# Kernel optimization log

Hardware: AMD Instinct MI355X
Metric: run time of the kernel (lower is better)

## Reference

```python
import jax, jax.numpy as jnp
import numpy as np
import math

B, N, HID, NH = 128, 512, 512, 8
DH = HID // NH  # d_heads = 64


def setup_inputs() -> dict:
    key = jax.random.key(0)
    ks = jax.random.split(key, 8)
    s = 0.05  # keep logits in a sane range
    h = jax.random.normal(ks[0], (B, N, HID), dtype=jnp.float32)
    lengths = jax.random.randint(ks[1], (B,), 1, N + 1, dtype=jnp.int32)
    w_q = jax.random.normal(ks[2], (HID, HID), dtype=jnp.float32) * s
    w_k = jax.random.normal(ks[3], (HID, HID), dtype=jnp.float32) * s
    w_v = jax.random.normal(ks[4], (HID, HID), dtype=jnp.float32) * s
    w_o = jax.random.normal(ks[5], (HID, HID), dtype=jnp.float32) * s
    w_seed_w = jax.random.normal(ks[6], (HID, 1), dtype=jnp.float32) * s  # Linear(1, k*hidden), k=1
    w_seed_b = jax.random.normal(ks[7], (HID,), dtype=jnp.float32) * s
    seed_vec = jnp.ones((1,), dtype=jnp.float32)
    return {"h": h, "lengths": lengths, "w_q": w_q, "w_k": w_k, "w_v": w_v,
            "w_o": w_o, "w_seed_w": w_seed_w, "w_seed_b": w_seed_b, "seed_vec": seed_vec}


def reference(h, lengths, w_q, w_k, w_v, w_o, w_seed_w, w_seed_b, seed_vec):
    # PMA with k=1 seed query. norm_features=False.
    # query = w_seed(seed_vec), same for every graph in the batch.
    query = w_seed_w @ seed_vec + w_seed_b            # [HID]
    q = (w_q @ query).reshape(NH, DH)                 # [NH, DH] (Linear: x @ W.T == W @ x for vector)
    # NOTE: original code computes w_k(v) but never uses it in attention; output
    # depends only on q and v (e = q * v summed over d_heads). We skip the dead compute.
    v = (h @ w_v.T).reshape(B, N, NH, DH)             # [B, N, NH, DH]
    # logits: e[b,h,n] = <q[h], v[b,n,h]> / sqrt(DH)
    e = jnp.einsum("hd,bnhd->bhn", q, v) / math.sqrt(DH)
    valid = jnp.arange(N)[None, :] < lengths[:, None]  # [B, N] ragged mask
    e = jnp.where(valid[:, None, :], e, -jnp.inf)
    alpha = jax.nn.softmax(e, axis=-1)                # [B, NH, N]; padded cols -> 0
    out_h = jnp.einsum("bhn,bnhd->bhd", alpha, v)     # [B, NH, DH]
    out = out_h.reshape(B, HID) @ w_o.T               # [B*k, HID], packed (k=1)
    alpha_out = alpha[..., None]                      # [B, NH, N, 1] matching torch permute
    return out, alpha_out
```

## Files before the change

### kernel.cpp

```cpp
#include <hip/hip_runtime.h>
#include <math.h>

constexpr int B = 128, N = 512, HID = 512, NH = 8, DH = 64;

__global__ __launch_bounds__(64) void k1_qk(
    const float* __restrict__ w_q, const float* __restrict__ w_v,
    const float* __restrict__ w_sw, const float* __restrict__ w_sb,
    const float* __restrict__ seed, float* __restrict__ qk)
{
    __shared__ __align__(16) float query_s[HID];
    __shared__ float q_s[DH];
    const int t  = threadIdx.x;
    const int h  = blockIdx.x >> 3;
    const int jc = blockIdx.x & 7;
    const float sv = seed[0];
    #pragma unroll
    for (int k = 0; k < 8; ++k) {
        const int j = t * 8 + k;
        query_s[j] = w_sw[j] * sv + w_sb[j];
    }
    __syncthreads();
    {
        const float* row = w_q + (size_t)(h * DH + t) * HID;
        float acc = 0.f;
        for (int j = 0; j < HID; j += 4) {
            const float4 wv = *(const float4*)(row + j);
            acc += wv.x * query_s[j]     + wv.y * query_s[j + 1]
                 + wv.z * query_s[j + 2] + wv.w * query_s[j + 3];
        }
        q_s[t] = acc;
    }
    __syncthreads();
    {
        const int j = jc * 64 + t;
        float acc = 0.f;
        for (int d = 0; d < DH; ++d)
            acc += q_s[d] * w_v[(size_t)(h * DH + d) * HID + j];
        qk[h * HID + j] = acc * 0.125f;
    }
}

__global__ __launch_bounds__(256) void ke_logits(
    const float* __restrict__ hbuf, const int* __restrict__ lengths,
    const float* __restrict__ qk, float* __restrict__ e_ws)
{
    const int t = threadIdx.x;
    const int l = t & 63;
    const int w = t >> 6;
    const int b = blockIdx.x >> 3;
    const int c = blockIdx.x & 7;
    const int n0 = c * 64;
    const int len = lengths[b];
    if (n0 >= len) return;

    float4 qlo[NH], qhi[NH];
    #pragma unroll
    for (int hh = 0; hh < NH; ++hh) {
        qlo[hh] = *(const float4*)&qk[hh * HID + l * 4];
        qhi[hh] = *(const float4*)&qk[hh * HID + 256 + l * 4];
    }

    const int nmax = min(n0 + 64, len);
    const float* hb = hbuf + (size_t)b * N * HID;
    const int hh_out = ((l & 1) << 2) | (l & 2) | ((l >> 2) & 1);

    for (int n = n0 + w; n < nmax; n += 4) {
        const float* row = hb + (size_t)n * HID;
        const float4 h0 = *(const float4*)(row + l * 4);
        const float4 h1 = *(const float4*)(row + 256 + l * 4);
        float v[NH];
        #pragma unroll
        for (int hh = 0; hh < NH; ++hh)
            v[hh] = h0.x * qlo[hh].x + h0.y * qlo[hh].y
                  + h0.z * qlo[hh].z + h0.w * qlo[hh].w
                  + h1.x * qhi[hh].x + h1.y * qhi[hh].y
                  + h1.z * qhi[hh].z + h1.w * qhi[hh].w;

        #pragma unroll
        for (int i = 0; i < 4; ++i) {
            const float ax = __shfl_xor(v[i], 1, 64);
            const float bx = __shfl_xor(v[i + 4], 1, 64);
            v[i] = (l & 1) ? (v[i + 4] + bx) : (v[i] + ax);
        }
        #pragma unroll
        for (int i = 0; i < 2; ++i) {
            const float ax = __shfl_xor(v[i], 2, 64);
            const float bx = __shfl_xor(v[i + 2], 2, 64);
            v[i] = (l & 2) ? (v[i + 2] + bx) : (v[i] + ax);
        }
        {
            const float ax = __shfl_xor(v[0], 4, 64);
            const float bx = __shfl_xor(v[1], 4, 64);
            v[0] = (l & 4) ? (v[1] + bx) : (v[0] + ax);
        }
        v[0] += __shfl_xor(v[0], 8, 64);
        v[0] += __shfl_xor(v[0], 16, 64);
        v[0] += __shfl_xor(v[0], 32, 64);

        if (l < 8)
            e_ws[(size_t)(b * NH + hh_out) * N + n] = v[0];
    }
}

__global__ __launch_bounds__(256) void ks_softmax(
    const float* __restrict__ e_ws, const int* __restrict__ lengths,
    float* __restrict__ alpha, float* __restrict__ al_t)
{
    const int b    = blockIdx.x >> 1;
    const int grp  = blockIdx.x & 1;
    const int lane = threadIdx.x & 63;
    const int hh   = grp * 4 + (threadIdx.x >> 6);
    const int len  = lengths[b];

    const float* e = e_ws + (size_t)(b * NH + hh) * N;
    float ev[8];
    float m = -3.0e38f;
    #pragma unroll
    for (int it = 0; it < 8; ++it) {
        const int n = it * 64 + lane;
        ev[it] = (n < len) ? e[n] : -3.0e38f;
        m = fmaxf(m, ev[it]);
    }
    #pragma unroll
    for (int off = 32; off; off >>= 1)
        m = fmaxf(m, __shfl_xor(m, off, 64));
    float s = 0.f;
    #pragma unroll
    for (int it = 0; it < 8; ++it) {
        ev[it] = __expf(ev[it] - m);
        s += ev[it];
    }
    #pragma unroll
    for (int off = 32; off; off >>= 1)
        s += __shfl_xor(s, off, 64);
    const float inv = 1.f / s;
    float* ao = alpha + (size_t)(b * NH + hh) * N;
    float* at = al_t + (size_t)b * N * NH + hh;
    #pragma unroll
    for (int it = 0; it < 8; ++it) {
        const int n   = it * 64 + lane;
        const float v = (n < len) ? ev[it] * inv : 0.f;
        ao[n]      = v;
        at[n * NH] = v;
    }
}

__global__ __launch_bounds__(256) void kc_ctx(
    const float* __restrict__ hbuf, const int* __restrict__ lengths,
    const float* __restrict__ al_t, float* __restrict__ ctxp)
{
    const int t   = threadIdx.x;
    const int b   = blockIdx.x >> 3;
    const int c   = blockIdx.x & 7;
    const int n0  = c * 64;
    const int g   = t >> 7;
    const int cq  = t & 127;
    const int len = lengths[b];
    const int nend = min(len - n0, 64);

    float4 acc[NH];
    #pragma unroll
    for (int hh = 0; hh < NH; ++hh) { acc[hh].x = acc[hh].y = acc[hh].z = acc[hh].w = 0.f; }

    const float* hb = hbuf + ((size_t)b * N + n0) * HID + cq * 4;
    const float* ap = al_t + ((size_t)b * N + n0) * NH;
    #pragma unroll 4
    for (int ln = g; ln < nend; ln += 2) {
        const float4 hv = *(const float4*)(hb + (size_t)ln * HID);
        const float* a = ap + ln * NH;
        acc[0].x += a[0] * hv.x; acc[0].y += a[0] * hv.y; acc[0].z += a[0] * hv.z; acc[0].w += a[0] * hv.w;
        acc[1].x += a[1] * hv.x; acc[1].y += a[1] * hv.y; acc[1].z += a[1] * hv.z; acc[1].w += a[1] * hv.w;
        acc[2].x += a[2] * hv.x; acc[2].y += a[2] * hv.y; acc[2].z += a[2] * hv.z; acc[2].w += a[2] * hv.w;
        acc[3].x += a[3] * hv.x; acc[3].y += a[3] * hv.y; acc[3].z += a[3] * hv.z; acc[3].w += a[3] * hv.w;
        acc[4].x += a[4] * hv.x; acc[4].y += a[4] * hv.y; acc[4].z += a[4] * hv.z; acc[4].w += a[4] * hv.w;
        acc[5].x += a[5] * hv.x; acc[5].y += a[5] * hv.y; acc[5].z += a[5] * hv.z; acc[5].w += a[5] * hv.w;
        acc[6].x += a[6] * hv.x; acc[6].y += a[6] * hv.y; acc[6].z += a[6] * hv.z; acc[6].w += a[6] * hv.w;
        acc[7].x += a[7] * hv.x; acc[7].y += a[7] * hv.y; acc[7].z += a[7] * hv.z; acc[7].w += a[7] * hv.w;
    }
    float* cp = ctxp + (size_t)(((b * 8 + c) * 2 + g) * NH) * HID + cq * 4;
    #pragma unroll
    for (int hh = 0; hh < NH; ++hh)
        *(float4*)(cp + (size_t)hh * HID) = acc[hh];
}

__global__ __launch_bounds__(256) void kd_out(
    const float* __restrict__ ctxp, const float* __restrict__ w_v,
    const float* __restrict__ w_o, float* __restrict__ out)
{
    __shared__ __align__(16) float ctx_s[NH * HID];
    __shared__ __align__(16) float oh_s[HID];
    const int t = threadIdx.x;
    const int b = blockIdx.x;
    const float* p0 = ctxp + (size_t)(b * 16) * NH * HID;
    for (int i = t; i < NH * HID; i += 256) {
        float s = 0.f;
        #pragma unroll
        for (int cc = 0; cc < 16; ++cc) s += p0[(size_t)cc * NH * HID + i];
        ctx_s[i] = s;
    }
    __syncthreads();
    #pragma unroll
    for (int rep = 0; rep < 2; ++rep) {
        const int p  = rep * 256 + t;
        const int hh = p >> 6;
        const float* wrow = w_v + (size_t)p * HID;
        float acc = 0.f;
        for (int j = 0; j < HID; j += 4) {
            const float4 wv = *(const float4*)(wrow + j);
            const float4 cv = *(const float4*)&ctx_s[hh * HID + j];
            acc += wv.x * cv.x + wv.y * cv.y + wv.z * cv.z + wv.w * cv.w;
        }
        oh_s[p] = acc;
    }
    __syncthreads();
    #pragma unroll
    for (int rep = 0; rep < 2; ++rep) {
        const int i = rep * 256 + t;
        const float* wrow = w_o + (size_t)i * HID;
        float acc = 0.f;
        for (int j = 0; j < HID; j += 4) {
            const float4 wv = *(const float4*)(wrow + j);
            const float4 ov = *(const float4*)&oh_s[j];
            acc += wv.x * ov.x + wv.y * ov.y + wv.z * ov.z + wv.w * ov.w;
        }
        out[(size_t)b * HID + i] = acc;
    }
}

extern "C" void kernel_launch(void* const* d_in, const int* in_sizes, int n_in,
                              void* d_out, int out_size, void* d_ws, size_t ws_size,
                              hipStream_t stream) {
    const float* h     = (const float*)d_in[0];
    const int*   lens  = (const int*)  d_in[1];
    const float* w_q   = (const float*)d_in[2];
    const float* w_v   = (const float*)d_in[4];
    const float* w_o   = (const float*)d_in[5];
    const float* w_sw  = (const float*)d_in[6];
    const float* w_sb  = (const float*)d_in[7];
    const float* seed  = (const float*)d_in[8];

    float* out   = (float*)d_out;
    float* alpha = out + (size_t)B * HID;

    float* ws   = (float*)d_ws;
    float* qk   = ws;
    float* e_ws = qk + NH * HID;
    float* al_t = e_ws + (size_t)B * NH * N;
    float* ctxp = al_t + (size_t)B * N * NH;

    hipLaunchKernelGGL(k1_qk,      dim3(64),    dim3(64),  0, stream,
                       w_q, w_v, w_sw, w_sb, seed, qk);
    hipLaunchKernelGGL(ke_logits,  dim3(B * 8), dim3(256), 0, stream,
                       h, lens, qk, e_ws);
    hipLaunchKernelGGL(ks_softmax, dim3(B * 2), dim3(256), 0, stream,
                       e_ws, lens, alpha, al_t);
    hipLaunchKernelGGL(kc_ctx,     dim3(B * 8), dim3(256), 0, stream,
                       h, lens, al_t, ctxp);
    hipLaunchKernelGGL(kd_out,     dim3(B),     dim3(256), 0, stream,
                       ctxp, w_v, w_o, out);
}
```

Before: 305.1 us.

## Reduce context with atomics and batch output projections across graphs

The logits kernel now processes two rows per iteration and interleaves their shuffle reductions to expose more instruction-level parallelism. It also zeroes a per-graph context buffer. The context kernel first reduces its two halves in shared memory and then atomically adds into that buffer, replacing the 16-way partial buffer. The final projection is split into two kernels that batch 16 graphs per block, so each weight row is reused across graphs instead of every graph reading the full w_v and w_o. In exchange it adds one extra launch, float atomic contention, and non-deterministic summation order.

Result: slower. 339.6 us (+11.3%).

```diff
diff --git a/kernel.cpp b/kernel.cpp
--- a/kernel.cpp
+++ b/kernel.cpp
@@ -40,9 +40,39 @@
     }
 }
 
+__device__ __forceinline__ void fold2(float va[NH], float vb[NH], int l,
+                                      float& ra, float& rb)
+{
+    #pragma unroll
+    for (int i = 0; i < 4; ++i) {
+        const float a0 = __shfl_xor(va[i], 1, 64), a1 = __shfl_xor(va[i + 4], 1, 64);
+        const float b0 = __shfl_xor(vb[i], 1, 64), b1 = __shfl_xor(vb[i + 4], 1, 64);
+        va[i] = (l & 1) ? (va[i + 4] + a1) : (va[i] + a0);
+        vb[i] = (l & 1) ? (vb[i + 4] + b1) : (vb[i] + b0);
+    }
+    #pragma unroll
+    for (int i = 0; i < 2; ++i) {
+        const float a0 = __shfl_xor(va[i], 2, 64), a1 = __shfl_xor(va[i + 2], 2, 64);
+        const float b0 = __shfl_xor(vb[i], 2, 64), b1 = __shfl_xor(vb[i + 2], 2, 64);
+        va[i] = (l & 2) ? (va[i + 2] + a1) : (va[i] + a0);
+        vb[i] = (l & 2) ? (vb[i + 2] + b1) : (vb[i] + b0);
+    }
+    {
+        const float a0 = __shfl_xor(va[0], 4, 64), a1 = __shfl_xor(va[1], 4, 64);
+        const float b0 = __shfl_xor(vb[0], 4, 64), b1 = __shfl_xor(vb[1], 4, 64);
+        va[0] = (l & 4) ? (va[1] + a1) : (va[0] + a0);
+        vb[0] = (l & 4) ? (vb[1] + b1) : (vb[0] + b0);
+    }
+    va[0] += __shfl_xor(va[0], 8, 64);  vb[0] += __shfl_xor(vb[0], 8, 64);
+    va[0] += __shfl_xor(va[0], 16, 64); vb[0] += __shfl_xor(vb[0], 16, 64);
+    va[0] += __shfl_xor(va[0], 32, 64); vb[0] += __shfl_xor(vb[0], 32, 64);
+    ra = va[0]; rb = vb[0];
+}
+
 __global__ __launch_bounds__(256) void ke_logits(
     const float* __restrict__ hbuf, const int* __restrict__ lengths,
-    const float* __restrict__ qk, float* __restrict__ e_ws)
+    const float* __restrict__ qk, float* __restrict__ e_ws,
+    float* __restrict__ ctx)
 {
     const int t = threadIdx.x;
     const int l = t & 63;
@@ -51,6 +81,12 @@
     const int c = blockIdx.x & 7;
     const int n0 = c * 64;
     const int len = lengths[b];
+
+    {
+        float* cz = ctx + (size_t)b * (NH * HID) + c * 512;
+        cz[t] = 0.f;
+        cz[t + 256] = 0.f;
+    }
     if (n0 >= len) return;
 
     float4 qlo[NH], qhi[NH];
@@ -64,41 +100,37 @@
     const float* hb = hbuf + (size_t)b * N * HID;
     const int hh_out = ((l & 1) << 2) | (l & 2) | ((l >> 2) & 1);
 
-    for (int n = n0 + w; n < nmax; n += 4) {
-        const float* row = hb + (size_t)n * HID;
-        const float4 h0 = *(const float4*)(row + l * 4);
-        const float4 h1 = *(const float4*)(row + 256 + l * 4);
-        float v[NH];
-        #pragma unroll
-        for (int hh = 0; hh < NH; ++hh)
-            v[hh] = h0.x * qlo[hh].x + h0.y * qlo[hh].y
-                  + h0.z * qlo[hh].z + h0.w * qlo[hh].w
-                  + h1.x * qhi[hh].x + h1.y * qhi[hh].y
-                  + h1.z * qhi[hh].z + h1.w * qhi[hh].w;
-
-        #pragma unroll
-        for (int i = 0; i < 4; ++i) {
-            const float ax = __shfl_xor(v[i], 1, 64);
-            const float bx = __shfl_xor(v[i + 4], 1, 64);
-            v[i] = (l & 1) ? (v[i + 4] + bx) : (v[i] + ax);
-        }
-        #pragma unroll
-        for (int i = 0; i < 2; ++i) {
-            const float ax = __shfl_xor(v[i], 2, 64);
-            const float bx = __shfl_xor(v[i + 2], 2, 64);
-            v[i] = (l & 2) ? (v[i + 2] + bx) : (v[i] + ax);
-        }
-        {
-            const float ax = __shfl_xor(v[0], 4, 64);
-            const float bx = __shfl_xor(v[1], 4, 64);
-            v[0] = (l & 4) ? (v[1] + bx) : (v[0] + ax);
-        }
-        v[0] += __shfl_xor(v[0], 8, 64);
-        v[0] += __shfl_xor(v[0], 16, 64);
-        v[0] += __shfl_xor(v[0], 32, 64);
-
-        if (l < 8)
-            e_ws[(size_t)(b * NH + hh_out) * N + n] = v[0];
+    for (int k = 0; k < 8; ++k) {
+        const int na = n0 + w + 8 * k;
+        if (na >= nmax) break;
+        const int nb = min(na + 4, nmax - 1);
+
+        const float* rowa = hb + (size_t)na * HID;
+        const float* rowb = hb + (size_t)nb * HID;
+        const float4 a0 = *(const float4*)(rowa + l * 4);
+        const float4 a1 = *(const float4*)(rowa + 256 + l * 4);
+        const float4 b0 = *(const float4*)(rowb + l * 4);
+        const float4 b1 = *(const float4*)(rowb + 256 + l * 4);
+
+        float va[NH], vb[NH];
+        #pragma unroll
+        for (int hh = 0; hh < NH; ++hh) {
+            va[hh] = a0.x * qlo[hh].x + a0.y * qlo[hh].y
+                   + a0.z * qlo[hh].z + a0.w * qlo[hh].w
+                   + a1.x * qhi[hh].x + a1.y * qhi[hh].y
+                   + a1.z * qhi[hh].z + a1.w * qhi[hh].w;
+            vb[hh] = b0.x * qlo[hh].x + b0.y * qlo[hh].y
+                   + b0.z * qlo[hh].z + b0.w * qlo[hh].w
+                   + b1.x * qhi[hh].x + b1.y * qhi[hh].y
+                   + b1.z * qhi[hh].z + b1.w * qhi[hh].w;
+        }
+        float ra, rb;
+        fold2(va, vb, l, ra, rb);
+        if (l < 8) {
+            e_ws[(size_t)(b * NH + hh_out) * N + na] = ra;
+            if (na + 4 < nmax)
+                e_ws[(size_t)(b * NH + hh_out) * N + nb] = rb;
+        }
     }
 }
 
@@ -147,8 +179,9 @@
 
 __global__ __launch_bounds__(256) void kc_ctx(
     const float* __restrict__ hbuf, const int* __restrict__ lengths,
-    const float* __restrict__ al_t, float* __restrict__ ctxp)
-{
+    const float* __restrict__ al_t, float* __restrict__ ctx)
+{
+    __shared__ __align__(16) float4 red[NH][128];
     const int t   = threadIdx.x;
     const int b   = blockIdx.x >> 3;
     const int c   = blockIdx.x & 7;
@@ -157,6 +190,7 @@
     const int cq  = t & 127;
     const int len = lengths[b];
     const int nend = min(len - n0, 64);
+    if (nend <= 0) return;
 
     float4 acc[NH];
     #pragma unroll
@@ -177,53 +211,79 @@
         acc[6].x += a[6] * hv.x; acc[6].y += a[6] * hv.y; acc[6].z += a[6] * hv.z; acc[6].w += a[6] * hv.w;
         acc[7].x += a[7] * hv.x; acc[7].y += a[7] * hv.y; acc[7].z += a[7] * hv.z; acc[7].w += a[7] * hv.w;
     }
-    float* cp = ctxp + (size_t)(((b * 8 + c) * 2 + g) * NH) * HID + cq * 4;
-    #pragma unroll
-    for (int hh = 0; hh < NH; ++hh)
-        *(float4*)(cp + (size_t)hh * HID) = acc[hh];
-}
-
-__global__ __launch_bounds__(256) void kd_out(
-    const float* __restrict__ ctxp, const float* __restrict__ w_v,
-    const float* __restrict__ w_o, float* __restrict__ out)
-{
-    __shared__ __align__(16) float ctx_s[NH * HID];
-    __shared__ __align__(16) float oh_s[HID];
-    const int t = threadIdx.x;
-    const int b = blockIdx.x;
-    const float* p0 = ctxp + (size_t)(b * 16) * NH * HID;
-    for (int i = t; i < NH * HID; i += 256) {
-        float s = 0.f;
-        #pragma unroll
-        for (int cc = 0; cc < 16; ++cc) s += p0[(size_t)cc * NH * HID + i];
-        ctx_s[i] = s;
+    if (g == 1) {
+        #pragma unroll
+        for (int hh = 0; hh < NH; ++hh) red[hh][cq] = acc[hh];
     }
     __syncthreads();
-    #pragma unroll
-    for (int rep = 0; rep < 2; ++rep) {
-        const int p  = rep * 256 + t;
-        const int hh = p >> 6;
-        const float* wrow = w_v + (size_t)p * HID;
-        float acc = 0.f;
-        for (int j = 0; j < HID; j += 4) {
-            const float4 wv = *(const float4*)(wrow + j);
-            const float4 cv = *(const float4*)&ctx_s[hh * HID + j];
-            acc += wv.x * cv.x + wv.y * cv.y + wv.z * cv.z + wv.w * cv.w;
-        }
-        oh_s[p] = acc;
-    }
-    __syncthreads();
-    #pragma unroll
-    for (int rep = 0; rep < 2; ++rep) {
-        const int i = rep * 256 + t;
-        const float* wrow = w_o + (size_t)i * HID;
-        float acc = 0.f;
-        for (int j = 0; j < HID; j += 4) {
-            const float4 wv = *(const float4*)(wrow + j);
-            const float4 ov = *(const float4*)&oh_s[j];
-            acc += wv.x * ov.x + wv.y * ov.y + wv.z * ov.z + wv.w * ov.w;
-        }
-        out[(size_t)b * HID + i] = acc;
+    if (g == 0) {
+        #pragma unroll
+        for (int hh = 0; hh < NH; ++hh) {
+            const float4 r = red[hh][cq];
+            float* dst = ctx + (size_t)b * (NH * HID) + hh * HID + cq * 4;
+            atomicAdd(dst + 0, acc[hh].x + r.x);
+            atomicAdd(dst + 1, acc[hh].y + r.y);
+            atomicAdd(dst + 2, acc[hh].z + r.z);
+            atomicAdd(dst + 3, acc[hh].w + r.w);
+        }
+    }
+}
+
+__global__ __launch_bounds__(256) void kd1_oh(
+    const float* __restrict__ ctx, const float* __restrict__ w_v,
+    float* __restrict__ oh)
+{
+    const int t  = threadIdx.x;
+    const int ht = blockIdx.x & 7;
+    const int bt = blockIdx.x >> 3;
+    const int d  = t & 63;
+    const int bs = t >> 6;
+    const int p  = ht * 64 + d;
+    const float* wrow = w_v + (size_t)p * HID;
+
+    float acc[4] = {0.f, 0.f, 0.f, 0.f};
+    for (int j = 0; j < HID; j += 4) {
+        const float4 wv = *(const float4*)(wrow + j);
+        #pragma unroll
+        for (int bi = 0; bi < 4; ++bi) {
+            const int bb = bt * 16 + bs * 4 + bi;
+            const float4 cv = *(const float4*)&ctx[(size_t)bb * (NH * HID) + ht * HID + j];
+            acc[bi] += wv.x * cv.x + wv.y * cv.y + wv.z * cv.z + wv.w * cv.w;
+        }
+    }
+    #pragma unroll
+    for (int bi = 0; bi < 4; ++bi) {
+        const int bb = bt * 16 + bs * 4 + bi;
+        oh[(size_t)bb * HID + p] = acc[bi];
+    }
+}
+
+__global__ __launch_bounds__(256) void kd2_out(
+    const float* __restrict__ oh, const float* __restrict__ w_o,
+    float* __restrict__ out)
+{
+    const int t  = threadIdx.x;
+    const int it = blockIdx.x & 7;
+    const int bt = blockIdx.x >> 3;
+    const int d  = t & 63;
+    const int bs = t >> 6;
+    const int i  = it * 64 + d;
+    const float* wrow = w_o + (size_t)i * HID;
+
+    float acc[4] = {0.f, 0.f, 0.f, 0.f};
+    for (int j = 0; j < HID; j += 4) {
+        const float4 wv = *(const float4*)(wrow + j);
+        #pragma unroll
+        for (int bi = 0; bi < 4; ++bi) {
+            const int bb = bt * 16 + bs * 4 + bi;
+            const float4 ov = *(const float4*)&oh[(size_t)bb * HID + j];
+            acc[bi] += wv.x * ov.x + wv.y * ov.y + wv.z * ov.z + wv.w * ov.w;
+        }
+    }
+    #pragma unroll
+    for (int bi = 0; bi < 4; ++bi) {
+        const int bb = bt * 16 + bs * 4 + bi;
+        out[(size_t)bb * HID + i] = acc[bi];
     }
 }
 
@@ -246,16 +306,19 @@
     float* qk   = ws;
     float* e_ws = qk + NH * HID;
     float* al_t = e_ws + (size_t)B * NH * N;
-    float* ctxp = al_t + (size_t)B * N * NH;
+    float* ctx  = al_t + (size_t)B * N * NH;
+    float* oh   = ctx + (size_t)B * NH * HID;
 
     hipLaunchKernelGGL(k1_qk,      dim3(64),    dim3(64),  0, stream,
                        w_q, w_v, w_sw, w_sb, seed, qk);
     hipLaunchKernelGGL(ke_logits,  dim3(B * 8), dim3(256), 0, stream,
-                       h, lens, qk, e_ws);
+                       h, lens, qk, e_ws, ctx);
     hipLaunchKernelGGL(ks_softmax, dim3(B * 2), dim3(256), 0, stream,
                        e_ws, lens, alpha, al_t);
     hipLaunchKernelGGL(kc_ctx,     dim3(B * 8), dim3(256), 0, stream,
-                       h, lens, al_t, ctxp);
-    hipLaunchKernelGGL(kd_out,     dim3(B),     dim3(256), 0, stream,
-                       ctxp, w_v, w_o, out);
-}
+                       h, lens, al_t, ctx);
+    hipLaunchKernelGGL(kd1_oh,     dim3(64),    dim3(256), 0, stream,
+                       ctx, w_v, oh);
+    hipLaunchKernelGGL(kd2_out,    dim3(64),    dim3(256), 0, stream,
+                       oh, w_o, out);
+}
```

## Reduce ctx partials in shared memory and batch output projections across graphs

Applied to the files above, without the earlier changes.

kc_ctx now sums its two row-group partials in shared memory before writing, which halves the partial-context buffer written and later read. The single per-graph output kernel is split into two kernels, w_v projection and then w_o projection. Each block handles 16 graphs and one 64-row slice of the weight, so every weight row loaded is reused across 4 graphs instead of being re-read for each graph. This adds one kernel launch, an intermediate global buffer, and fewer blocks (64) in the projection stages.

After: 291.0 us. 4.6% less time.

```diff
diff --git a/kernel.cpp b/kernel.cpp
--- a/kernel.cpp
+++ b/kernel.cpp
@@ -149,6 +149,7 @@
     const float* __restrict__ hbuf, const int* __restrict__ lengths,
     const float* __restrict__ al_t, float* __restrict__ ctxp)
 {
+    __shared__ __align__(16) float4 red[NH][128];
     const int t   = threadIdx.x;
     const int b   = blockIdx.x >> 3;
     const int c   = blockIdx.x & 7;
@@ -177,53 +178,103 @@
         acc[6].x += a[6] * hv.x; acc[6].y += a[6] * hv.y; acc[6].z += a[6] * hv.z; acc[6].w += a[6] * hv.w;
         acc[7].x += a[7] * hv.x; acc[7].y += a[7] * hv.y; acc[7].z += a[7] * hv.z; acc[7].w += a[7] * hv.w;
     }
-    float* cp = ctxp + (size_t)(((b * 8 + c) * 2 + g) * NH) * HID + cq * 4;
-    #pragma unroll
-    for (int hh = 0; hh < NH; ++hh)
-        *(float4*)(cp + (size_t)hh * HID) = acc[hh];
-}
-
-__global__ __launch_bounds__(256) void kd_out(
+    if (g == 1) {
+        #pragma unroll
+        for (int hh = 0; hh < NH; ++hh) red[hh][cq] = acc[hh];
+    }
+    __syncthreads();
+    if (g == 0) {
+        float* cp = ctxp + (size_t)((b * 8 + c) * NH) * HID + cq * 4;
+        #pragma unroll
+        for (int hh = 0; hh < NH; ++hh) {
+            const float4 r = red[hh][cq];
+            float4 o;
+            o.x = acc[hh].x + r.x; o.y = acc[hh].y + r.y;
+            o.z = acc[hh].z + r.z; o.w = acc[hh].w + r.w;
+            *(float4*)(cp + (size_t)hh * HID) = o;
+        }
+    }
+}
+
+__global__ __launch_bounds__(256) void kd1_oh(
     const float* __restrict__ ctxp, const float* __restrict__ w_v,
-    const float* __restrict__ w_o, float* __restrict__ out)
-{
-    __shared__ __align__(16) float ctx_s[NH * HID];
-    __shared__ __align__(16) float oh_s[HID];
-    const int t = threadIdx.x;
-    const int b = blockIdx.x;
-    const float* p0 = ctxp + (size_t)(b * 16) * NH * HID;
-    for (int i = t; i < NH * HID; i += 256) {
-        float s = 0.f;
-        #pragma unroll
-        for (int cc = 0; cc < 16; ++cc) s += p0[(size_t)cc * NH * HID + i];
-        ctx_s[i] = s;
-    }
-    __syncthreads();
-    #pragma unroll
-    for (int rep = 0; rep < 2; ++rep) {
-        const int p  = rep * 256 + t;
-        const int hh = p >> 6;
-        const float* wrow = w_v + (size_t)p * HID;
-        float acc = 0.f;
-        for (int j = 0; j < HID; j += 4) {
-            const float4 wv = *(const float4*)(wrow + j);
-            const float4 cv = *(const float4*)&ctx_s[hh * HID + j];
-            acc += wv.x * cv.x + wv.y * cv.y + wv.z * cv.z + wv.w * cv.w;
-        }
-        oh_s[p] = acc;
-    }
-    __syncthreads();
-    #pragma unroll
-    for (int rep = 0; rep < 2; ++rep) {
-        const int i = rep * 256 + t;
-        const float* wrow = w_o + (size_t)i * HID;
-        float acc = 0.f;
-        for (int j = 0; j < HID; j += 4) {
-            const float4 wv = *(const float4*)(wrow + j);
-            const float4 ov = *(const float4*)&oh_s[j];
-            acc += wv.x * ov.x + wv.y * ov.y + wv.z * ov.z + wv.w * ov.w;
-        }
-        out[(size_t)b * HID + i] = acc;
+    float* __restrict__ oh)
+{
+    __shared__ __align__(16) float ctx_s[16][HID];
+    const int t  = threadIdx.x;
+    const int ht = blockIdx.x & 7;
+    const int bt = blockIdx.x >> 3;
+
+    for (int idx = t; idx < 16 * 128; idx += 256) {
+        const int bb_l = idx >> 7;
+        const int j4   = idx & 127;
+        const int bb   = bt * 16 + bb_l;
+        const float* p0 = ctxp + ((size_t)(bb * 8) * NH + ht) * HID + j4 * 4;
+        float4 s = {0.f, 0.f, 0.f, 0.f};
+        #pragma unroll
+        for (int cc = 0; cc < 8; ++cc) {
+            const float4 v = *(const float4*)(p0 + (size_t)cc * NH * HID);
+            s.x += v.x; s.y += v.y; s.z += v.z; s.w += v.w;
+        }
+        *(float4*)&ctx_s[bb_l][j4 * 4] = s;
+    }
+    __syncthreads();
+
+    const int d  = t & 63;
+    const int bs = t >> 6;
+    const int p  = ht * 64 + d;
+    const float* wrow = w_v + (size_t)p * HID;
+    float acc[4] = {0.f, 0.f, 0.f, 0.f};
+    for (int j = 0; j < HID; j += 4) {
+        const float4 wv = *(const float4*)(wrow + j);
+        #pragma unroll
+        for (int bi = 0; bi < 4; ++bi) {
+            const float4 cv = *(const float4*)&ctx_s[bs * 4 + bi][j];
+            acc[bi] += wv.x * cv.x + wv.y * cv.y + wv.z * cv.z + wv.w * cv.w;
+        }
+    }
+    #pragma unroll
+    for (int bi = 0; bi < 4; ++bi) {
+        const int bb = bt * 16 + bs * 4 + bi;
+        oh[(size_t)bb * HID + p] = acc[bi];
+    }
+}
+
+__global__ __launch_bounds__(256) void kd2_out(
+    const float* __restrict__ oh, const float* __restrict__ w_o,
+    float* __restrict__ out)
+{
+    __shared__ __align__(16) float oh_s[16][HID];
+    const int t  = threadIdx.x;
+    const int it = blockIdx.x & 7;
+    const int bt = blockIdx.x >> 3;
+
+    for (int idx = t; idx < 16 * 128; idx += 256) {
+        const int bb_l = idx >> 7;
+        const int j4   = idx & 127;
+        const int bb   = bt * 16 + bb_l;
+        *(float4*)&oh_s[bb_l][j4 * 4] =
+            *(const float4*)&oh[(size_t)bb * HID + j4 * 4];
+    }
+    __syncthreads();
+
+    const int d  = t & 63;
+    const int bs = t >> 6;
+    const int i  = it * 64 + d;
+    const float* wrow = w_o + (size_t)i * HID;
+    float acc[4] = {0.f, 0.f, 0.f, 0.f};
+    for (int j = 0; j < HID; j += 4) {
+        const float4 wv = *(const float4*)(wrow + j);
+        #pragma unroll
+        for (int bi = 0; bi < 4; ++bi) {
+            const float4 ov = *(const float4*)&oh_s[bs * 4 + bi][j];
+            acc[bi] += wv.x * ov.x + wv.y * ov.y + wv.z * ov.z + wv.w * ov.w;
+        }
+    }
+    #pragma unroll
+    for (int bi = 0; bi < 4; ++bi) {
+        const int bb = bt * 16 + bs * 4 + bi;
+        out[(size_t)bb * HID + i] = acc[bi];
     }
 }
 
@@ -247,6 +298,7 @@
     float* e_ws = qk + NH * HID;
     float* al_t = e_ws + (size_t)B * NH * N;
     float* ctxp = al_t + (size_t)B * N * NH;
+    float* oh   = ctxp + (size_t)B * 8 * NH * HID;
 
     hipLaunchKernelGGL(k1_qk,      dim3(64),    dim3(64),  0, stream,
                        w_q, w_v, w_sw, w_sb, seed, qk);
@@ -256,6 +308,8 @@
                        e_ws, lens, alpha, al_t);
     hipLaunchKernelGGL(kc_ctx,     dim3(B * 8), dim3(256), 0, stream,
                        h, lens, al_t, ctxp);
-    hipLaunchKernelGGL(kd_out,     dim3(B),     dim3(256), 0, stream,
-                       ctxp, w_v, w_o, out);
-}
+    hipLaunchKernelGGL(kd1_oh,     dim3(64),    dim3(256), 0, stream,
+                       ctxp, w_v, oh);
+    hipLaunchKernelGGL(kd2_out,    dim3(64),    dim3(256), 0, stream,
+                       oh, w_o, out);
+}
```
